# Performance work log

Measured on AMD Instinct MI355X. Metric: run time of the kernel, lower is better.

Reference implementation:

```python
import jax, jax.numpy as jnp
import numpy as np

F = 64  # dim_features
DIM_TASK = 32


def setup_inputs() -> dict:
    key = jax.random.key(0)
    ks = jax.random.split(key, 16)
    n_state, n_task, n_actor = 65536, 32768, 32768
    E_st, E_ta = 2_000_000, 1_000_000
    inp = {
        'x_state': jax.random.normal(ks[0], (n_state, F), jnp.float32),
        'x_task': jax.random.normal(ks[1], (n_task, F), jnp.float32),
        'x_actor': jax.random.normal(ks[2], (n_actor, F), jnp.float32),
        'edge_attr': jax.random.normal(ks[3], (E_st, 2), jnp.float32),
        # GINEConv edge linear: Linear(2 -> F)
        'We': jax.random.normal(ks[4], (2, F), jnp.float32) * 0.5,
        'be': jnp.zeros((F,), jnp.float32),
        # GinStandardMLP: Linear(F,F) -> ReLU -> Linear(F,F)
        'W1a': jax.random.normal(ks[5], (F, F), jnp.float32) / np.sqrt(F),
        'b1a': jnp.zeros((F,), jnp.float32),
        'W1b': jax.random.normal(ks[6], (F, F), jnp.float32) / np.sqrt(F),
        'b1b': jnp.zeros((F,), jnp.float32),
        # UnactivatedMLP: Linear(F,F) -> ReLU -> Linear(F,1)
        'W2a': jax.random.normal(ks[7], (F, F), jnp.float32) / np.sqrt(F),
        'b2a': jnp.zeros((F,), jnp.float32),
        'W2b': jax.random.normal(ks[8], (F, 1), jnp.float32) / np.sqrt(F),
        'b2b': jnp.zeros((1,), jnp.float32),
        'src_st': jax.random.randint(ks[9], (E_st,), 0, n_state, jnp.int32),
        'dst_st': jax.random.randint(ks[10], (E_st,), 0, n_task, jnp.int32),
        'src_ta': jax.random.randint(ks[11], (E_ta,), 0, n_task, jnp.int32),
        'dst_ta': jax.random.randint(ks[12], (E_ta,), 0, n_actor, jnp.int32),
    }
    return inp


def reference(x_state, x_task, x_actor, edge_attr, We, be, W1a, b1a, W1b, b1b,
              W2a, b2a, W2b, b2b, src_st, dst_st, src_ta, dst_ta):
    n_task = x_task.shape[0]
    n_actor = x_actor.shape[0]
    # --- GINEConv (eps=0): agg_i = sum_e relu(x_src[e] + lin(edge_attr[e])) ---
    msg = jax.nn.relu(x_state[src_st] + edge_attr @ We + be)  # [E_st, F]
    agg = jax.ops.segment_sum(msg, dst_st, num_segments=n_task)  # [n_task, F]
    h = x_task + agg  # (1+eps)*x_r + agg, eps=0
    # GinStandardMLP: Linear-ReLU-Linear
    x1 = jax.nn.relu(h @ W1a + b1a) @ W1b + b1b  # [n_task, F]
    # --- GINConv (eps=0): agg2_i = sum_e x1[src[e]] ---
    agg2 = jax.ops.segment_sum(x1[src_ta], dst_ta, num_segments=n_actor)  # [n_actor, F]
    h2 = x_actor + agg2
    # UnactivatedMLP: Linear-ReLU-Linear -> 1
    logits = jax.nn.relu(h2 @ W2a + b2a) @ W2b + b2b  # [n_actor, 1]
    return logits.reshape(-1, DIM_TASK)
```

## Files before the change

### kernel.cpp

```cpp
#include <hip/hip_runtime.h>

#define F 64
#define TILE 4096
#define NB 1024
#define ROWSB 32
#define CAP1 2560
#define CAP2 1408

typedef __attribute__((ext_vector_type(8))) short bf8;
typedef __attribute__((ext_vector_type(4))) float f4;
typedef __attribute__((ext_vector_type(2))) float fl2;

__device__ __forceinline__ unsigned short f2bf(float f) {
    unsigned u = __float_as_uint(f);
    unsigned r = u + 0x7fffu + ((u >> 16) & 1u);
    return (unsigned short)(r >> 16);
}
__device__ __forceinline__ float bf2f(unsigned short h) {
    return __uint_as_float((unsigned)h << 16);
}
__device__ __forceinline__ fl2 unpack2(unsigned d) {
    fl2 r;
    r.x = __uint_as_float(d << 16);
    r.y = __uint_as_float(d & 0xffff0000u);
    return r;
}

__global__ __launch_bounds__(1024) void prep_kernel(
    const float4* __restrict__ xs4, ushort4* __restrict__ xsb4, int n4,
    const int* __restrict__ src1, const int* __restrict__ dst1,
    const float* __restrict__ ea, int E1,
    int* __restrict__ cur1, uint2* __restrict__ keyA1,
    const int* __restrict__ src2, const int* __restrict__ dst2, int E2,
    int* __restrict__ cur2, unsigned* __restrict__ keyA2,
    int nCvt, int nBin1)
{
    __shared__ uint2 stage[TILE];
    __shared__ int hist[NB], scanb[NB], lstart[NB], lcur[NB], gbase[NB];
    int bid = blockIdx.x;
    int tid = threadIdx.x;

    if (bid < nCvt) {
        int i = bid * 1024 + tid;
        if (i < n4) {
            float4 v = xs4[i];
            ushort4 o;
            o.x = f2bf(v.x); o.y = f2bf(v.y); o.z = f2bf(v.z); o.w = f2bf(v.w);
            xsb4[i] = o;
        }
        return;
    }

    if (bid < nCvt + nBin1) {
        int base = (bid - nCvt) * TILE;
        int cnt = min(TILE, E1 - base);
        hist[tid] = 0;
        __syncthreads();
        int myb[4];
        #pragma unroll
        for (int j = 0; j < 4; ++j) {
            int idx = tid + 1024 * j;
            if (idx < cnt) {
                int b = dst1[base + idx] >> 5;
                myb[j] = b;
                atomicAdd(&hist[b], 1);
            } else myb[j] = -1;
        }
        __syncthreads();
        int c = hist[tid];
        gbase[tid] = CAP1 * tid + atomicAdd(&cur1[tid], c);
        scanb[tid] = c;
        __syncthreads();
        for (int off = 1; off < NB; off <<= 1) {
            int u = (tid >= off) ? scanb[tid - off] : 0;
            __syncthreads();
            scanb[tid] += u;
            __syncthreads();
        }
        int excl = scanb[tid] - c;
        lstart[tid] = excl;
        lcur[tid] = excl;
        __syncthreads();
        #pragma unroll
        for (int j = 0; j < 4; ++j) {
            int idx = tid + 1024 * j;
            if (idx < cnt) {
                int b = myb[j];
                int p = atomicAdd(&lcur[b], 1);
                float2 e2 = ((const float2* __restrict__)ea)[base + idx];
                unsigned sd = ((unsigned)src1[base + idx] << 16) | (unsigned)dst1[base + idx];
                unsigned pk = ((unsigned)f2bf(e2.y) << 16) | (unsigned)f2bf(e2.x);
                stage[p] = make_uint2(sd, pk);
            }
        }
        __syncthreads();
        #pragma unroll
        for (int j = 0; j < 4; ++j) {
            int p = tid + 1024 * j;
            if (p < cnt) {
                uint2 f = stage[p];
                int b = (int)(f.x & 0xffffu) >> 5;
                keyA1[gbase[b] + (p - lstart[b])] = f;
            }
        }
        return;
    }

    {
        unsigned* ustage = (unsigned*)stage;
        int base = (bid - nCvt - nBin1) * TILE;
        int cnt = min(TILE, E2 - base);
        hist[tid] = 0;
        __syncthreads();
        int myb[4];
        #pragma unroll
        for (int j = 0; j < 4; ++j) {
            int idx = tid + 1024 * j;
            if (idx < cnt) {
                int b = dst2[base + idx] >> 5;
                myb[j] = b;
                atomicAdd(&hist[b], 1);
            } else myb[j] = -1;
        }
        __syncthreads();
        int c = hist[tid];
        gbase[tid] = CAP2 * tid + atomicAdd(&cur2[tid], c);
        scanb[tid] = c;
        __syncthreads();
        for (int off = 1; off < NB; off <<= 1) {
            int u = (tid >= off) ? scanb[tid - off] : 0;
            __syncthreads();
            scanb[tid] += u;
            __syncthreads();
        }
        int excl = scanb[tid] - c;
        lstart[tid] = excl;
        lcur[tid] = excl;
        __syncthreads();
        #pragma unroll
        for (int j = 0; j < 4; ++j) {
            int idx = tid + 1024 * j;
            if (idx < cnt) {
                int b = myb[j];
                int p = atomicAdd(&lcur[b], 1);
                ustage[p] = ((unsigned)src2[base + idx] << 16) | (unsigned)dst2[base + idx];
            }
        }
        __syncthreads();
        #pragma unroll
        for (int j = 0; j < 4; ++j) {
            int p = tid + 1024 * j;
            if (p < cnt) {
                unsigned f = ustage[p];
                int b = (int)(f & 0xffffu) >> 5;
                keyA2[gbase[b] + (p - lstart[b])] = f;
            }
        }
    }
}

__global__ __launch_bounds__(512) void sg1_kernel(
    const uint2* __restrict__ keyA,
    const ushort* __restrict__ xsb,
    const float* __restrict__ x_task,
    const float* __restrict__ We, const float* __restrict__ be,
    const int* __restrict__ gcursor,
    float* __restrict__ hout, int n)
{
    __shared__ uint2 lpay[CAP1];
    __shared__ int hh[ROWSB], rst[ROWSB], cur[ROWSB];
    int tid = threadIdx.x;
    int b = blockIdx.x;
    int cnt = min(gcursor[b], CAP1);
    const uint2* ka = keyA + (size_t)b * CAP1;

    if (tid < ROWSB) hh[tid] = 0;
    __syncthreads();

    uint2 myk[5];
    #pragma unroll
    for (int j = 0; j < 5; ++j) {
        int idx = tid + 512 * j;
        if (idx < cnt) {
            myk[j] = ka[idx];
            atomicAdd(&hh[myk[j].x & 31u], 1);
        }
    }
    __syncthreads();
    if (tid < ROWSB) cur[tid] = hh[tid];
    __syncthreads();
    for (int off = 1; off < ROWSB; off <<= 1) {
        int u = (tid < ROWSB && tid >= off) ? cur[tid - off] : 0;
        __syncthreads();
        if (tid < ROWSB) cur[tid] += u;
        __syncthreads();
    }
    if (tid < ROWSB) {
        int excl = cur[tid] - hh[tid];
        rst[tid] = excl;
        cur[tid] = excl;
    }
    __syncthreads();
    #pragma unroll
    for (int j = 0; j < 5; ++j) {
        int idx = tid + 512 * j;
        if (idx < cnt) {
            int p = atomicAdd(&cur[myk[j].x & 31u], 1);
            lpay[p] = myk[j];
        }
    }
    __syncthreads();

    int wave = tid >> 6, lane = tid & 63;
    int q = lane & 7, g = lane >> 3;
    int gid = (wave << 3) | g;
    int r   = gid >> 1;
    int h   = gid & 1;
    int row = b * ROWSB + r;

    fl2 w0p[4], w1p[4], bbp[4];
    {
        float4 a0 = ((const float4* __restrict__)We)[q * 2];
        float4 a1 = ((const float4* __restrict__)We)[q * 2 + 1];
        float4 c0 = ((const float4* __restrict__)(We + F))[q * 2];
        float4 c1 = ((const float4* __restrict__)(We + F))[q * 2 + 1];
        float4 d0 = ((const float4* __restrict__)be)[q * 2];
        float4 d1 = ((const float4* __restrict__)be)[q * 2 + 1];
        w0p[0] = (fl2){a0.x, a0.y}; w0p[1] = (fl2){a0.z, a0.w};
        w0p[2] = (fl2){a1.x, a1.y}; w0p[3] = (fl2){a1.z, a1.w};
        w1p[0] = (fl2){c0.x, c0.y}; w1p[1] = (fl2){c0.z, c0.w};
        w1p[2] = (fl2){c1.x, c1.y}; w1p[3] = (fl2){c1.z, c1.w};
        bbp[0] = (fl2){d0.x, d0.y}; bbp[1] = (fl2){d0.z, d0.w};
        bbp[2] = (fl2){d1.x, d1.y}; bbp[3] = (fl2){d1.z, d1.w};
    }
    const fl2 zero2 = {0.f, 0.f};

    int c  = hh[r];
    int m0 = (c + 1) >> 1;
    int sh = rst[r] + (h ? m0 : 0);
    int m  = h ? (c - m0) : m0;

    fl2 acc2[4];
    #pragma unroll
    for (int p = 0; p < 4; ++p) acc2[p] = zero2;

    unsigned pk0 = 0, pk1 = 0, pk2 = 0, pk3 = 0;
    uint4 xw0 = {0,0,0,0}, xw1 = {0,0,0,0}, xw2 = {0,0,0,0}, xw3 = {0,0,0,0};

    #define SG1_LOAD(J, K)                                                          \
    if ((K) < m) {                                                                  \
        uint2 t = lpay[sh + (K)];                                                   \
        pk##J = t.y;                                                                \
        xw##J = ((const uint4* __restrict__)(xsb + ((size_t)(t.x >> 16) << 6)))[q]; \
    }

    #define SG1_COMP(PK, XW)                                                        \
    {                                                                               \
        fl2 ex = {__uint_as_float((PK) << 16), __uint_as_float((PK) << 16)};        \
        fl2 ey = {__uint_as_float((PK) & 0xffff0000u),                              \
                  __uint_as_float((PK) & 0xffff0000u)};                             \
        fl2 cc, t2;                                                                 \
        cc = __builtin_elementwise_fma(ey, w1p[0], bbp[0]);                         \
        cc = __builtin_elementwise_fma(ex, w0p[0], cc);                             \
        t2 = unpack2((XW).x) + cc;                                                  \
        acc2[0] += __builtin_elementwise_max(t2, zero2);                            \
        cc = __builtin_elementwise_fma(ey, w1p[1], bbp[1]);                         \
        cc = __builtin_elementwise_fma(ex, w0p[1], cc);                             \
        t2 = unpack2((XW).y) + cc;                                                  \
        acc2[1] += __builtin_elementwise_max(t2, zero2);                            \
        cc = __builtin_elementwise_fma(ey, w1p[2], bbp[2]);                         \
        cc = __builtin_elementwise_fma(ex, w0p[2], cc);                             \
        t2 = unpack2((XW).z) + cc;                                                  \
        acc2[2] += __builtin_elementwise_max(t2, zero2);                            \
        cc = __builtin_elementwise_fma(ey, w1p[3], bbp[3]);                         \
        cc = __builtin_elementwise_fma(ex, w0p[3], cc);                             \
        t2 = unpack2((XW).w) + cc;                                                  \
        acc2[3] += __builtin_elementwise_max(t2, zero2);                            \
    }

    SG1_LOAD(0, 0)
    SG1_LOAD(1, 1)
    SG1_LOAD(2, 2)
    SG1_LOAD(3, 3)
    int i = 0;
    for (; i + 4 <= m; i += 4) {
        SG1_COMP(pk0, xw0) SG1_LOAD(0, i + 4)
        SG1_COMP(pk1, xw1) SG1_LOAD(1, i + 5)
        SG1_COMP(pk2, xw2) SG1_LOAD(2, i + 6)
        SG1_COMP(pk3, xw3) SG1_LOAD(3, i + 7)
    }
    if (i < m)     SG1_COMP(pk0, xw0)
    if (i + 1 < m) SG1_COMP(pk1, xw1)
    if (i + 2 < m) SG1_COMP(pk2, xw2)
    #undef SG1_LOAD
    #undef SG1_COMP

    float acc[8];
    #pragma unroll
    for (int p = 0; p < 4; ++p) { acc[2 * p] = acc2[p].x; acc[2 * p + 1] = acc2[p].y; }
    #pragma unroll
    for (int j = 0; j < 8; ++j) acc[j] += __shfl_xor(acc[j], 8);

    if (h == 0 && row < n) {
        const float4* xt = (const float4* __restrict__)(x_task + (size_t)row * F + q * 8);
        float4 t0 = xt[0], t1 = xt[1];
        float4 o0, o1;
        o0.x = acc[0] + t0.x; o0.y = acc[1] + t0.y; o0.z = acc[2] + t0.z; o0.w = acc[3] + t0.w;
        o1.x = acc[4] + t1.x; o1.y = acc[5] + t1.y; o1.z = acc[6] + t1.z; o1.w = acc[7] + t1.w;
        float4* hp = (float4*)(hout + (size_t)row * F + q * 8);
        hp[0] = o0; hp[1] = o1;
    }
}

__global__ __launch_bounds__(256) void mlp1_kernel(
    const float* __restrict__ hin,
    const float* __restrict__ W1a, const float* __restrict__ b1a,
    const float* __restrict__ W1b, const float* __restrict__ b1b,
    ushort* __restrict__ x1b, int n)
{
    __shared__ float ldsH[4][16 * 68];
    int tid = threadIdx.x;
    int wave = tid >> 6, lane = tid & 63;
    int quad = lane >> 4, col = lane & 15;
    int rowbase = blockIdx.x * 64 + wave * 16;
    if (rowbase >= n) return;
    float* ltile = ldsH[wave];

    bf8 Wah[2][4], Wal[2][4], Wbh[2][4], Wbl[2][4];
    float ba1[4], bb1[4];
    #pragma unroll
    for (int kh = 0; kh < 2; ++kh)
        #pragma unroll
        for (int c = 0; c < 4; ++c) {
            bf8 th, tl, sh, sl;
            #pragma unroll
            for (int j = 0; j < 8; ++j) {
                int k = kh * 32 + quad * 8 + j;
                float wa = W1a[k * F + c * 16 + col];
                unsigned short h1 = f2bf(wa);
                th[j] = (short)h1; tl[j] = (short)f2bf(wa - bf2f(h1));
                float wb = W1b[k * F + c * 16 + col];
                unsigned short h2 = f2bf(wb);
                sh[j] = (short)h2; sl[j] = (short)f2bf(wb - bf2f(h2));
            }
            Wah[kh][c] = th; Wal[kh][c] = tl;
            Wbh[kh][c] = sh; Wbl[kh][c] = sl;
        }
    #pragma unroll
    for (int c = 0; c < 4; ++c) { ba1[c] = b1a[c * 16 + col]; bb1[c] = b1b[c * 16 + col]; }

    const float* hrow = hin + (size_t)(rowbase + col) * F + quad * 8;
    bf8 Ah[2], Al[2];
    #pragma unroll
    for (int kh = 0; kh < 2; ++kh) {
        bf8 th, tl;
        #pragma unroll
        for (int j = 0; j < 8; ++j) {
            float a = hrow[kh * 32 + j];
            unsigned short h1 = f2bf(a);
            th[j] = (short)h1; tl[j] = (short)f2bf(a - bf2f(h1));
        }
        Ah[kh] = th; Al[kh] = tl;
    }

    #pragma unroll
    for (int c = 0; c < 4; ++c) {
        f4 acc = {0.f, 0.f, 0.f, 0.f};
        #pragma unroll
        for (int kh = 0; kh < 2; ++kh) {
            acc = __builtin_amdgcn_mfma_f32_16x16x32_bf16(Ah[kh], Wah[kh][c], acc, 0, 0, 0);
            acc = __builtin_amdgcn_mfma_f32_16x16x32_bf16(Ah[kh], Wal[kh][c], acc, 0, 0, 0);
            acc = __builtin_amdgcn_mfma_f32_16x16x32_bf16(Al[kh], Wah[kh][c], acc, 0, 0, 0);
        }
        #pragma unroll
        for (int r = 0; r < 4; ++r)
            ltile[(quad * 4 + r) * 68 + c * 16 + col] = fmaxf(acc[r] + ba1[c], 0.f);
    }
    bf8 A2h[2], A2l[2];
    #pragma unroll
    for (int kh = 0; kh < 2; ++kh) {
        bf8 th, tl;
        #pragma unroll
        for (int j = 0; j < 8; ++j) {
            float a = ltile[col * 68 + kh * 32 + quad * 8 + j];
            unsigned short h1 = f2bf(a);
            th[j] = (short)h1; tl[j] = (short)f2bf(a - bf2f(h1));
        }
        A2h[kh] = th; A2l[kh] = tl;
    }
    #pragma unroll
    for (int c = 0; c < 4; ++c) {
        f4 acc = {0.f, 0.f, 0.f, 0.f};
        #pragma unroll
        for (int kh = 0; kh < 2; ++kh) {
            acc = __builtin_amdgcn_mfma_f32_16x16x32_bf16(A2h[kh], Wbh[kh][c], acc, 0, 0, 0);
            acc = __builtin_amdgcn_mfma_f32_16x16x32_bf16(A2h[kh], Wbl[kh][c], acc, 0, 0, 0);
            acc = __builtin_amdgcn_mfma_f32_16x16x32_bf16(A2l[kh], Wbh[kh][c], acc, 0, 0, 0);
        }
        #pragma unroll
        for (int r = 0; r < 4; ++r)
            ltile[(quad * 4 + r) * 68 + c * 16 + col] = acc[r] + bb1[c];
    }
    int rr = lane >> 2, cc = (lane & 3) * 16;
    unsigned o[8];
    #pragma unroll
    for (int j = 0; j < 8; ++j) {
        unsigned lo = f2bf(ltile[rr * 68 + cc + 2 * j]);
        unsigned hi = f2bf(ltile[rr * 68 + cc + 2 * j + 1]);
        o[j] = lo | (hi << 16);
    }
    uint4* dst = (uint4*)(x1b + (size_t)(rowbase + rr) * F + cc);
    dst[0] = make_uint4(o[0], o[1], o[2], o[3]);
    dst[1] = make_uint4(o[4], o[5], o[6], o[7]);
}

__global__ __launch_bounds__(512) void sg2_kernel(
    const unsigned* __restrict__ keyA,
    const ushort* __restrict__ x1b,
    const float* __restrict__ x_actor,
    const int* __restrict__ gcursor,
    float* __restrict__ h2out, int n)
{
    __shared__ unsigned lpay[CAP2];
    __shared__ int hh[ROWSB], rst[ROWSB], cur[ROWSB];
    int tid = threadIdx.x;
    int b = blockIdx.x;
    int cnt = min(gcursor[b], CAP2);
    const unsigned* ka = keyA + (size_t)b * CAP2;

    if (tid < ROWSB) hh[tid] = 0;
    __syncthreads();

    unsigned myk[3];
    #pragma unroll
    for (int j = 0; j < 3; ++j) {
        int idx = tid + 512 * j;
        if (idx < cnt) {
            myk[j] = ka[idx];
            atomicAdd(&hh[myk[j] & 31u], 1);
        }
    }
    __syncthreads();
    if (tid < ROWSB) cur[tid] = hh[tid];
    __syncthreads();
    for (int off = 1; off < ROWSB; off <<= 1) {
        int u = (tid < ROWSB && tid >= off) ? cur[tid - off] : 0;
        __syncthreads();
        if (tid < ROWSB) cur[tid] += u;
        __syncthreads();
    }
    if (tid < ROWSB) {
        int excl = cur[tid] - hh[tid];
        rst[tid] = excl;
        cur[tid] = excl;
    }
    __syncthreads();
    #pragma unroll
    for (int j = 0; j < 3; ++j) {
        int idx = tid + 512 * j;
        if (idx < cnt) {
            int p = atomicAdd(&cur[myk[j] & 31u], 1);
            lpay[p] = myk[j];
        }
    }
    __syncthreads();

    int wave = tid >> 6, lane = tid & 63;
    int q = lane & 7, g = lane >> 3;
    int gid = (wave << 3) | g;
    int r   = gid >> 1;
    int h   = gid & 1;
    int row = b * ROWSB + r;
    const fl2 zero2 = {0.f, 0.f};

    int c  = hh[r];
    int m0 = (c + 1) >> 1;
    int sh = rst[r] + (h ? m0 : 0);
    int m  = h ? (c - m0) : m0;

    fl2 acc2[4];
    #pragma unroll
    for (int p = 0; p < 4; ++p) acc2[p] = zero2;

    uint4 xw0 = {0,0,0,0}, xw1 = {0,0,0,0}, xw2 = {0,0,0,0}, xw3 = {0,0,0,0};

    #define SG2_LOAD(J, K)                                                          \
    if ((K) < m) {                                                                  \
        unsigned t = lpay[sh + (K)];                                                \
        xw##J = ((const uint4* __restrict__)(x1b + ((size_t)(t >> 16) << 6)))[q];   \
    }

    #define SG2_COMP(XW)                                                            \
    {                                                                               \
        acc2[0] += unpack2((XW).x);                                                 \
        acc2[1] += unpack2((XW).y);                                                 \
        acc2[2] += unpack2((XW).z);                                                 \
        acc2[3] += unpack2((XW).w);                                                 \
    }

    SG2_LOAD(0, 0)
    SG2_LOAD(1, 1)
    SG2_LOAD(2, 2)
    SG2_LOAD(3, 3)
    int i = 0;
    for (; i + 4 <= m; i += 4) {
        SG2_COMP(xw0) SG2_LOAD(0, i + 4)
        SG2_COMP(xw1) SG2_LOAD(1, i + 5)
        SG2_COMP(xw2) SG2_LOAD(2, i + 6)
        SG2_COMP(xw3) SG2_LOAD(3, i + 7)
    }
    if (i < m)     SG2_COMP(xw0)
    if (i + 1 < m) SG2_COMP(xw1)
    if (i + 2 < m) SG2_COMP(xw2)
    #undef SG2_LOAD
    #undef SG2_COMP

    float acc[8];
    #pragma unroll
    for (int p = 0; p < 4; ++p) { acc[2 * p] = acc2[p].x; acc[2 * p + 1] = acc2[p].y; }
    #pragma unroll
    for (int j = 0; j < 8; ++j) acc[j] += __shfl_xor(acc[j], 8);

    if (h == 0 && row < n) {
        const float4* xt = (const float4* __restrict__)(x_actor + (size_t)row * F + q * 8);
        float4 t0 = xt[0], t1 = xt[1];
        float4 o0, o1;
        o0.x = acc[0] + t0.x; o0.y = acc[1] + t0.y; o0.z = acc[2] + t0.z; o0.w = acc[3] + t0.w;
        o1.x = acc[4] + t1.x; o1.y = acc[5] + t1.y; o1.z = acc[6] + t1.z; o1.w = acc[7] + t1.w;
        float4* hp = (float4*)(h2out + (size_t)row * F + q * 8);
        hp[0] = o0; hp[1] = o1;
    }
}

__global__ __launch_bounds__(256) void mlp2_kernel(
    const float* __restrict__ h2in,
    const float* __restrict__ W2a, const float* __restrict__ b2a,
    const float* __restrict__ W2b, const float* __restrict__ b2b,
    float* __restrict__ out, int n)
{
    int tid = threadIdx.x;
    int wave = tid >> 6, lane = tid & 63;
    int quad = lane >> 4, col = lane & 15;
    int rowbase = blockIdx.x * 64 + wave * 16;
    if (rowbase >= n) return;

    bf8 Wah[2][4], Wal[2][4];
    float ba1[4], wo[4];
    #pragma unroll
    for (int kh = 0; kh < 2; ++kh)
        #pragma unroll
        for (int c = 0; c < 4; ++c) {
            bf8 th, tl;
            #pragma unroll
            for (int j = 0; j < 8; ++j) {
                int k = kh * 32 + quad * 8 + j;
                float w = W2a[k * F + c * 16 + col];
                unsigned short h1 = f2bf(w);
                th[j] = (short)h1; tl[j] = (short)f2bf(w - bf2f(h1));
            }
            Wah[kh][c] = th; Wal[kh][c] = tl;
        }
    #pragma unroll
    for (int c = 0; c < 4; ++c) { ba1[c] = b2a[c * 16 + col]; wo[c] = W2b[c * 16 + col]; }
    float bias2 = b2b[0];

    const float* hrow = h2in + (size_t)(rowbase + col) * F + quad * 8;
    bf8 Ah[2], Al[2];
    #pragma unroll
    for (int kh = 0; kh < 2; ++kh) {
        bf8 th, tl;
        #pragma unroll
        for (int j = 0; j < 8; ++j) {
            float a = hrow[kh * 32 + j];
            unsigned short h1 = f2bf(a);
            th[j] = (short)h1; tl[j] = (short)f2bf(a - bf2f(h1));
        }
        Ah[kh] = th; Al[kh] = tl;
    }

    float partial[4] = {0.f, 0.f, 0.f, 0.f};
    #pragma unroll
    for (int c = 0; c < 4; ++c) {
        f4 acc = {0.f, 0.f, 0.f, 0.f};
        #pragma unroll
        for (int kh = 0; kh < 2; ++kh) {
            acc = __builtin_amdgcn_mfma_f32_16x16x32_bf16(Ah[kh], Wah[kh][c], acc, 0, 0, 0);
            acc = __builtin_amdgcn_mfma_f32_16x16x32_bf16(Ah[kh], Wal[kh][c], acc, 0, 0, 0);
            acc = __builtin_amdgcn_mfma_f32_16x16x32_bf16(Al[kh], Wah[kh][c], acc, 0, 0, 0);
        }
        #pragma unroll
        for (int r = 0; r < 4; ++r)
            partial[r] += fmaxf(acc[r] + ba1[c], 0.f) * wo[c];
    }
    #pragma unroll
    for (int off = 1; off < 16; off <<= 1)
        #pragma unroll
        for (int r = 0; r < 4; ++r)
            partial[r] += __shfl_xor(partial[r], off);
    if (col == 0) {
        #pragma unroll
        for (int r = 0; r < 4; ++r)
            out[rowbase + quad * 4 + r] = partial[r] + bias2;
    }
}

extern "C" void kernel_launch(void* const* d_in, const int* in_sizes, int n_in,
                              void* d_out, int out_size, void* d_ws, size_t ws_size,
                              hipStream_t stream)
{
    const float* x_state   = (const float*)d_in[0];
    const float* x_task    = (const float*)d_in[1];
    const float* x_actor   = (const float*)d_in[2];
    const float* edge_attr = (const float*)d_in[3];
    const float* We        = (const float*)d_in[4];
    const float* be        = (const float*)d_in[5];
    const float* W1a       = (const float*)d_in[6];
    const float* b1a       = (const float*)d_in[7];
    const float* W1b       = (const float*)d_in[8];
    const float* b1b       = (const float*)d_in[9];
    const float* W2a       = (const float*)d_in[10];
    const float* b2a       = (const float*)d_in[11];
    const float* W2b       = (const float*)d_in[12];
    const float* b2b       = (const float*)d_in[13];
    const int*   src_st    = (const int*)d_in[14];
    const int*   dst_st    = (const int*)d_in[15];
    const int*   src_ta    = (const int*)d_in[16];
    const int*   dst_ta    = (const int*)d_in[17];

    int n_state = in_sizes[0] / F;
    int n_task  = in_sizes[1] / F;
    int n_actor = in_sizes[2] / F;
    int E_st    = in_sizes[14];
    int E_ta    = in_sizes[16];

    ushort*   x1b   = (ushort*)d_ws;
    float*    hbig  = (float*)(x1b + (size_t)n_task * F);
    ushort*   xsb   = (ushort*)(hbig + (size_t)n_task * F);
    uint2*    keyA1 = (uint2*)(xsb + (size_t)n_state * F);
    unsigned* keyA2 = (unsigned*)(keyA1 + (size_t)NB * CAP1);
    int*      cur1  = (int*)(keyA2 + (size_t)NB * CAP2);
    int*      cur2  = cur1 + NB;

    int n4    = n_state * F / 4;
    int nCvt  = (n4 + 1023) / 1024;
    int nBin1 = (E_st + TILE - 1) / TILE;
    int nBin2 = (E_ta + TILE - 1) / TILE;

    hipMemsetAsync(cur1, 0, 2 * NB * sizeof(int), stream);
    prep_kernel<<<nCvt + nBin1 + nBin2, 1024, 0, stream>>>(
        (const float4*)x_state, (ushort4*)xsb, n4,
        src_st, dst_st, edge_attr, E_st, cur1, keyA1,
        src_ta, dst_ta, E_ta, cur2, keyA2,
        nCvt, nBin1);
    sg1_kernel<<<NB, 512, 0, stream>>>(
        keyA1, xsb, x_task, We, be, cur1, hbig, n_task);
    mlp1_kernel<<<(n_task + 63) / 64, 256, 0, stream>>>(
        hbig, W1a, b1a, W1b, b1b, x1b, n_task);
    sg2_kernel<<<NB, 512, 0, stream>>>(
        keyA2, x1b, x_actor, cur2, hbig, n_actor);
    mlp2_kernel<<<(n_actor + 63) / 64, 256, 0, stream>>>(
        hbig, W2a, b2a, W2b, b2b, (float*)d_out, n_actor);
}
```

Baseline: 224.8 us.

## Use wave-shuffle scans, larger bin tiles, and reorder prep blocks

The 1024-entry shared-memory Hillis-Steele scan with many barriers is replaced by a wave-level shuffle scan plus a small cross-wave scan. The per-row 32-entry scans in the scatter-gather kernels get the same treatment. The binning tile doubles to 8192 edges per block, and edge fields are loaded once into registers before the histogram. The binning blocks now come before the conversion blocks in the grid, so the long-running binning work is scheduled first. The costs are higher register pressure from holding eight edges per thread and more shared memory for the larger staging buffer.

```diff
diff --git a/kernel.cpp b/kernel.cpp
--- a/kernel.cpp
+++ b/kernel.cpp
@@ -1,7 +1,7 @@
 #include <hip/hip_runtime.h>
 
 #define F 64
-#define TILE 4096
+#define TILE 8192
 #define NB 1024
 #define ROWSB 32
 #define CAP1 2560
@@ -24,6 +24,30 @@
     r.x = __uint_as_float(d << 16);
     r.y = __uint_as_float(d & 0xffff0000u);
     return r;
+}
+
+__device__ __forceinline__ int block_scan_1024(int c, int tid, int* scratch) {
+    int lane = tid & 63, wv = tid >> 6;
+    int s = c;
+    #pragma unroll
+    for (int off = 1; off < 64; off <<= 1) {
+        int u = __shfl_up(s, off);
+        if (lane >= off) s += u;
+    }
+    if (lane == 63) scratch[wv] = s;
+    __syncthreads();
+    if (tid < 64) {
+        int ws = (tid < 16) ? scratch[tid] : 0;
+        int t = ws;
+        #pragma unroll
+        for (int off = 1; off < 16; off <<= 1) {
+            int u = __shfl_up(t, off);
+            if (tid >= off) t += u;
+        }
+        if (tid < 16) scratch[16 + tid] = t - ws;
+    }
+    __syncthreads();
+    return s - c + scratch[16 + wv];
 }
 
 __global__ __launch_bounds__(1024) void prep_kernel(
@@ -33,128 +57,112 @@
     int* __restrict__ cur1, uint2* __restrict__ keyA1,
     const int* __restrict__ src2, const int* __restrict__ dst2, int E2,
     int* __restrict__ cur2, unsigned* __restrict__ keyA2,
-    int nCvt, int nBin1)
+    int nBin1, int nBin2)
 {
     __shared__ uint2 stage[TILE];
-    __shared__ int hist[NB], scanb[NB], lstart[NB], lcur[NB], gbase[NB];
+    __shared__ int hist[NB], lcur[NB], comb[NB];
+    __shared__ int scratch[32];
     int bid = blockIdx.x;
     int tid = threadIdx.x;
 
-    if (bid < nCvt) {
-        int i = bid * 1024 + tid;
+    if (bid < nBin1) {
+        int base = bid * TILE;
+        int cnt = min(TILE, E1 - base);
+        hist[tid] = 0;
+        __syncthreads();
+        int myb[8]; unsigned msd[8], mpk[8];
+        #pragma unroll
+        for (int j = 0; j < 8; ++j) {
+            int idx = tid + 1024 * j;
+            if (idx < cnt) {
+                int d = dst1[base + idx];
+                int s = src1[base + idx];
+                float2 e2 = ((const float2* __restrict__)ea)[base + idx];
+                myb[j] = d >> 5;
+                msd[j] = ((unsigned)s << 16) | (unsigned)d;
+                mpk[j] = ((unsigned)f2bf(e2.y) << 16) | (unsigned)f2bf(e2.x);
+                atomicAdd(&hist[myb[j]], 1);
+            } else myb[j] = -1;
+        }
+        __syncthreads();
+        int c = hist[tid];
+        int gb = CAP1 * tid + atomicAdd(&cur1[tid], c);
+        int excl = block_scan_1024(c, tid, scratch);
+        comb[tid] = gb - excl;
+        lcur[tid] = excl;
+        __syncthreads();
+        #pragma unroll
+        for (int j = 0; j < 8; ++j) {
+            if (myb[j] >= 0) {
+                int p = atomicAdd(&lcur[myb[j]], 1);
+                stage[p] = make_uint2(msd[j], mpk[j]);
+            }
+        }
+        __syncthreads();
+        #pragma unroll
+        for (int j = 0; j < 8; ++j) {
+            int p = tid + 1024 * j;
+            if (p < cnt) {
+                uint2 f = stage[p];
+                int b = (int)(f.x & 0xffffu) >> 5;
+                keyA1[comb[b] + p] = f;
+            }
+        }
+        return;
+    }
+
+    if (bid < nBin1 + nBin2) {
+        unsigned* ustage = (unsigned*)stage;
+        int base = (bid - nBin1) * TILE;
+        int cnt = min(TILE, E2 - base);
+        hist[tid] = 0;
+        __syncthreads();
+        int myb[8]; unsigned msd[8];
+        #pragma unroll
+        for (int j = 0; j < 8; ++j) {
+            int idx = tid + 1024 * j;
+            if (idx < cnt) {
+                int d = dst2[base + idx];
+                int s = src2[base + idx];
+                myb[j] = d >> 5;
+                msd[j] = ((unsigned)s << 16) | (unsigned)d;
+                atomicAdd(&hist[myb[j]], 1);
+            } else myb[j] = -1;
+        }
+        __syncthreads();
+        int c = hist[tid];
+        int gb = CAP2 * tid + atomicAdd(&cur2[tid], c);
+        int excl = block_scan_1024(c, tid, scratch);
+        comb[tid] = gb - excl;
+        lcur[tid] = excl;
+        __syncthreads();
+        #pragma unroll
+        for (int j = 0; j < 8; ++j) {
+            if (myb[j] >= 0) {
+                int p = atomicAdd(&lcur[myb[j]], 1);
+                ustage[p] = msd[j];
+            }
+        }
+        __syncthreads();
+        #pragma unroll
+        for (int j = 0; j < 8; ++j) {
+            int p = tid + 1024 * j;
+            if (p < cnt) {
+                unsigned f = ustage[p];
+                int b = (int)(f & 0xffffu) >> 5;
+                keyA2[comb[b] + p] = f;
+            }
+        }
+        return;
+    }
+
+    {
+        int i = (bid - nBin1 - nBin2) * 1024 + tid;
         if (i < n4) {
             float4 v = xs4[i];
             ushort4 o;
             o.x = f2bf(v.x); o.y = f2bf(v.y); o.z = f2bf(v.z); o.w = f2bf(v.w);
             xsb4[i] = o;
-        }
-        return;
-    }
-
-    if (bid < nCvt + nBin1) {
-        int base = (bid - nCvt) * TILE;
-        int cnt = min(TILE, E1 - base);
-        hist[tid] = 0;
-        __syncthreads();
-        int myb[4];
-        #pragma unroll
-        for (int j = 0; j < 4; ++j) {
-            int idx = tid + 1024 * j;
-            if (idx < cnt) {
-                int b = dst1[base + idx] >> 5;
-                myb[j] = b;
-                atomicAdd(&hist[b], 1);
-            } else myb[j] = -1;
-        }
-        __syncthreads();
-        int c = hist[tid];
-        gbase[tid] = CAP1 * tid + atomicAdd(&cur1[tid], c);
-        scanb[tid] = c;
-        __syncthreads();
-        for (int off = 1; off < NB; off <<= 1) {
-            int u = (tid >= off) ? scanb[tid - off] : 0;
-            __syncthreads();
-            scanb[tid] += u;
-            __syncthreads();
-        }
-        int excl = scanb[tid] - c;
-        lstart[tid] = excl;
-        lcur[tid] = excl;
-        __syncthreads();
-        #pragma unroll
-        for (int j = 0; j < 4; ++j) {
-            int idx = tid + 1024 * j;
-            if (idx < cnt) {
-                int b = myb[j];
-                int p = atomicAdd(&lcur[b], 1);
-                float2 e2 = ((const float2* __restrict__)ea)[base + idx];
-                unsigned sd = ((unsigned)src1[base + idx] << 16) | (unsigned)dst1[base + idx];
-                unsigned pk = ((unsigned)f2bf(e2.y) << 16) | (unsigned)f2bf(e2.x);
-                stage[p] = make_uint2(sd, pk);
-            }
-        }
-        __syncthreads();
-        #pragma unroll
-        for (int j = 0; j < 4; ++j) {
-            int p = tid + 1024 * j;
-            if (p < cnt) {
-                uint2 f = stage[p];
-                int b = (int)(f.x & 0xffffu) >> 5;
-                keyA1[gbase[b] + (p - lstart[b])] = f;
-            }
-        }
-        return;
-    }
-
-    {
-        unsigned* ustage = (unsigned*)stage;
-        int base = (bid - nCvt - nBin1) * TILE;
-        int cnt = min(TILE, E2 - base);
-        hist[tid] = 0;
-        __syncthreads();
-        int myb[4];
-        #pragma unroll
-        for (int j = 0; j < 4; ++j) {
-            int idx = tid + 1024 * j;
-            if (idx < cnt) {
-                int b = dst2[base + idx] >> 5;
-                myb[j] = b;
-                atomicAdd(&hist[b], 1);
-            } else myb[j] = -1;
-        }
-        __syncthreads();
-        int c = hist[tid];
-        gbase[tid] = CAP2 * tid + atomicAdd(&cur2[tid], c);
-        scanb[tid] = c;
-        __syncthreads();
-        for (int off = 1; off < NB; off <<= 1) {
-            int u = (tid >= off) ? scanb[tid - off] : 0;
-            __syncthreads();
-            scanb[tid] += u;
-            __syncthreads();
-        }
-        int excl = scanb[tid] - c;
-        lstart[tid] = excl;
-        lcur[tid] = excl;
-        __syncthreads();
-        #pragma unroll
-        for (int j = 0; j < 4; ++j) {
-            int idx = tid + 1024 * j;
-            if (idx < cnt) {
-                int b = myb[j];
-                int p = atomicAdd(&lcur[b], 1);
-                ustage[p] = ((unsigned)src2[base + idx] << 16) | (unsigned)dst2[base + idx];
-            }
-        }
-        __syncthreads();
-        #pragma unroll
-        for (int j = 0; j < 4; ++j) {
-            int p = tid + 1024 * j;
-            if (p < cnt) {
-                unsigned f = ustage[p];
-                int b = (int)(f & 0xffffu) >> 5;
-                keyA2[gbase[b] + (p - lstart[b])] = f;
-            }
         }
     }
 }
@@ -174,31 +182,29 @@
     int cnt = min(gcursor[b], CAP1);
     const uint2* ka = keyA + (size_t)b * CAP1;
 
-    if (tid < ROWSB) hh[tid] = 0;
-    __syncthreads();
-
     uint2 myk[5];
     #pragma unroll
     for (int j = 0; j < 5; ++j) {
         int idx = tid + 512 * j;
-        if (idx < cnt) {
-            myk[j] = ka[idx];
-            atomicAdd(&hh[myk[j].x & 31u], 1);
-        }
-    }
-    __syncthreads();
-    if (tid < ROWSB) cur[tid] = hh[tid];
-    __syncthreads();
-    for (int off = 1; off < ROWSB; off <<= 1) {
-        int u = (tid < ROWSB && tid >= off) ? cur[tid - off] : 0;
-        __syncthreads();
-        if (tid < ROWSB) cur[tid] += u;
-        __syncthreads();
-    }
-    if (tid < ROWSB) {
-        int excl = cur[tid] - hh[tid];
-        rst[tid] = excl;
-        cur[tid] = excl;
+        if (idx < cnt) myk[j] = ka[idx];
+    }
+    if (tid < ROWSB) hh[tid] = 0;
+    __syncthreads();
+    #pragma unroll
+    for (int j = 0; j < 5; ++j) {
+        int idx = tid + 512 * j;
+        if (idx < cnt) atomicAdd(&hh[myk[j].x & 31u], 1);
+    }
+    __syncthreads();
+    if (tid < 64) {
+        int cc = (tid < ROWSB) ? hh[tid] : 0;
+        int s = cc;
+        #pragma unroll
+        for (int off = 1; off < ROWSB; off <<= 1) {
+            int u = __shfl_up(s, off);
+            if (tid >= off) s += u;
+        }
+        if (tid < ROWSB) { rst[tid] = s - cc; cur[tid] = s - cc; }
     }
     __syncthreads();
     #pragma unroll
@@ -428,31 +434,29 @@
     int cnt = min(gcursor[b], CAP2);
     const unsigned* ka = keyA + (size_t)b * CAP2;
 
-    if (tid < ROWSB) hh[tid] = 0;
-    __syncthreads();
-
     unsigned myk[3];
     #pragma unroll
     for (int j = 0; j < 3; ++j) {
         int idx = tid + 512 * j;
-        if (idx < cnt) {
-            myk[j] = ka[idx];
-            atomicAdd(&hh[myk[j] & 31u], 1);
-        }
-    }
-    __syncthreads();
-    if (tid < ROWSB) cur[tid] = hh[tid];
-    __syncthreads();
-    for (int off = 1; off < ROWSB; off <<= 1) {
-        int u = (tid < ROWSB && tid >= off) ? cur[tid - off] : 0;
-        __syncthreads();
-        if (tid < ROWSB) cur[tid] += u;
-        __syncthreads();
-    }
-    if (tid < ROWSB) {
-        int excl = cur[tid] - hh[tid];
-        rst[tid] = excl;
-        cur[tid] = excl;
+        if (idx < cnt) myk[j] = ka[idx];
+    }
+    if (tid < ROWSB) hh[tid] = 0;
+    __syncthreads();
+    #pragma unroll
+    for (int j = 0; j < 3; ++j) {
+        int idx = tid + 512 * j;
+        if (idx < cnt) atomicAdd(&hh[myk[j] & 31u], 1);
+    }
+    __syncthreads();
+    if (tid < 64) {
+        int cc = (tid < ROWSB) ? hh[tid] : 0;
+        int s = cc;
+        #pragma unroll
+        for (int off = 1; off < ROWSB; off <<= 1) {
+            int u = __shfl_up(s, off);
+            if (tid >= off) s += u;
+        }
+        if (tid < ROWSB) { rst[tid] = s - cc; cur[tid] = s - cc; }
     }
     __syncthreads();
     #pragma unroll
@@ -647,11 +651,11 @@
     int nBin2 = (E_ta + TILE - 1) / TILE;
 
     hipMemsetAsync(cur1, 0, 2 * NB * sizeof(int), stream);
-    prep_kernel<<<nCvt + nBin1 + nBin2, 1024, 0, stream>>>(
+    prep_kernel<<<nBin1 + nBin2 + nCvt, 1024, 0, stream>>>(
         (const float4*)x_state, (ushort4*)xsb, n4,
         src_st, dst_st, edge_attr, E_st, cur1, keyA1,
         src_ta, dst_ta, E_ta, cur2, keyA2,
-        nCvt, nBin1);
+        nBin1, nBin2);
     sg1_kernel<<<NB, 512, 0, stream>>>(
         keyA1, xsb, x_task, We, be, cur1, hbig, n_task);
     mlp1_kernel<<<(n_task + 63) / 64, 256, 0, stream>>>(
```

Result: faster. 203.1 us (-9.6%).
